# Kernel optimization log

Measured on AMD Instinct MI355X. Metric: run time of the kernel, lower is better.

## Reference

```python
import jax, jax.numpy as jnp
import numpy as np
import math

NUM_HEADS = 16
NUM_KV_HEADS = 4
HEAD_DIM = 128
HIDDEN = 2048
ROPE_BASE = 10000.0


def setup_inputs() -> dict:
    key = jax.random.key(0)
    ks = jax.random.split(key, 6)
    B, S = 1, 4096
    hidden_states = jax.random.normal(ks[0], (B, S, HIDDEN), dtype=jnp.float32)
    attention_mask = jnp.ones((B, S), dtype=jnp.int32)
    position_ids = jnp.broadcast_to(jnp.arange(S, dtype=jnp.int32)[None, :], (B, S))
    sc = 1.0 / math.sqrt(HIDDEN)
    wq = jax.random.normal(ks[1], (HIDDEN, NUM_HEADS * HEAD_DIM), dtype=jnp.float32) * sc
    wk = jax.random.normal(ks[2], (HIDDEN, NUM_KV_HEADS * HEAD_DIM), dtype=jnp.float32) * sc
    wv = jax.random.normal(ks[3], (HIDDEN, NUM_KV_HEADS * HEAD_DIM), dtype=jnp.float32) * sc
    wo = jax.random.normal(ks[4], (NUM_HEADS * HEAD_DIM, HIDDEN), dtype=jnp.float32) * sc
    return {"hidden_states": hidden_states, "attention_mask": attention_mask,
            "position_ids": position_ids, "wq": wq, "wk": wk, "wv": wv, "wo": wo}


def _rotate_half(x):
    x1, x2 = jnp.split(x, 2, axis=-1)
    return jnp.concatenate((-x2, x1), axis=-1)


def _rope_tables(seq_len, dtype):
    inv_freq = 1.0 / (ROPE_BASE ** (jnp.arange(0, HEAD_DIM, 2, dtype=jnp.float32) / HEAD_DIM))
    t = jnp.arange(seq_len, dtype=jnp.float32)
    freqs = jnp.outer(t, inv_freq)                       # [S, hd/2]
    emb = jnp.concatenate((freqs, freqs), axis=-1)       # [S, hd]
    return jnp.cos(emb).astype(dtype), jnp.sin(emb).astype(dtype)


def reference(hidden_states, attention_mask, position_ids, wq, wk, wv, wo):
    B, S, _ = hidden_states.shape
    dtype = hidden_states.dtype
    # projections -> [B, H, S, hd]
    q = (hidden_states @ wq).reshape(B, S, NUM_HEADS, HEAD_DIM).transpose(0, 2, 1, 3)
    k = (hidden_states @ wk).reshape(B, S, NUM_KV_HEADS, HEAD_DIM).transpose(0, 2, 1, 3)
    v = (hidden_states @ wv).reshape(B, S, NUM_KV_HEADS, HEAD_DIM).transpose(0, 2, 1, 3)
    # RoPE
    cos_t, sin_t = _rope_tables(S, dtype)
    cos = cos_t[position_ids][:, None]                   # [B,1,S,hd]
    sin = sin_t[position_ids][:, None]
    q = q * cos + _rotate_half(q) * sin
    k = k * cos + _rotate_half(k) * sin
    # GQA repeat
    n_rep = NUM_HEADS // NUM_KV_HEADS
    k = jnp.repeat(k, n_rep, axis=1)
    v = jnp.repeat(v, n_rep, axis=1)
    # scores + causal mask + padding mask
    scores = jnp.einsum('bhqd,bhkd->bhqk', q, k) / math.sqrt(HEAD_DIM)
    neg = jnp.finfo(scores.dtype).min
    causal = jnp.triu(jnp.full((S, S), neg, dtype=scores.dtype), k=1)
    scores = scores + causal[None, None]
    pad = (1.0 - attention_mask.astype(scores.dtype))[:, None, None, :] * neg
    scores = scores + pad
    attn = jax.nn.softmax(scores.astype(jnp.float32), axis=-1).astype(dtype)
    out = jnp.einsum('bhqk,bhkd->bhqd', attn, v)
    out = out.transpose(0, 2, 1, 3).reshape(B, S, NUM_HEADS * HEAD_DIM)
    return out @ wo
```

## Files before the change

kernel.cpp:

```cpp
#include <hip/hip_runtime.h>
#include <cstdint>
#include <cstddef>

typedef unsigned short ushort_t;
typedef short    bf16x8 __attribute__((ext_vector_type(8)));
typedef float    f32x4  __attribute__((ext_vector_type(4)));
typedef uint4    __attribute__((may_alias)) uint4_a;
typedef ushort4  __attribute__((may_alias)) ushort4_a;
typedef float4   __attribute__((may_alias)) float4_a;
typedef unsigned __attribute__((may_alias)) uint_a;

constexpr int SEQ = 4096, HID = 2048, NHEADS = 16, NKVH = 4, HDIM = 128;
constexpr int QD  = NHEADS * HDIM;
constexpr int KVD = NKVH * HDIM;
constexpr int KVL = 2 * KVD;

static __device__ __forceinline__ float bf2f(ushort_t u) {
    return __uint_as_float(((unsigned)u) << 16);
}
static __device__ __forceinline__ ushort_t f2bf(float f) {
    unsigned x = __float_as_uint(f);
    unsigned r = x + 0x7FFFu + ((x >> 16) & 1u);
    return (ushort_t)(r >> 16);
}
static __device__ __forceinline__ unsigned pack2(float lo, float hi) {
    return (unsigned)f2bf(lo) | ((unsigned)f2bf(hi) << 16);
}

static __device__ __forceinline__ void gld16(const ushort_t* g, ushort_t* l) {
    __builtin_amdgcn_global_load_lds(
        (const __attribute__((address_space(1))) unsigned*)g,
        (__attribute__((address_space(3))) unsigned*)l, 16, 0, 0);
}

__global__ __launch_bounds__(256) void cast_f32_bf16(
    const float* __restrict__ in, ushort_t* __restrict__ out, int n)
{
    int i = (blockIdx.x * 256 + threadIdx.x) * 8;
    if (i >= n) return;
    float4 a = *(const float4_a*)(in + i);
    float4 b = *(const float4_a*)(in + i + 4);
    uint4 o;
    o.x = pack2(a.x, a.y); o.y = pack2(a.z, a.w);
    o.z = pack2(b.x, b.y); o.w = pack2(b.z, b.w);
    *(uint4_a*)(out + i) = o;
}

__global__ __launch_bounds__(256) void transpose_cast(
    const float* __restrict__ W, ushort_t* __restrict__ WT, int K, int N)
{
    __shared__ float tl[32][36];
    const int k0 = blockIdx.x * 32, n0 = blockIdx.y * 32;
    const int t  = threadIdx.x;
    {
        int i = t >> 3, jb = (t & 7) * 4;
        *(float4_a*)&tl[i][jb] = *(const float4_a*)(W + (size_t)(k0 + i) * N + n0 + jb);
    }
    __syncthreads();
    {
        int n = t >> 3, kb = (t & 7) * 4;
        ushort4 o;
        o.x = f2bf(tl[kb + 0][n]); o.y = f2bf(tl[kb + 1][n]);
        o.z = f2bf(tl[kb + 2][n]); o.w = f2bf(tl[kb + 3][n]);
        *(ushort4_a*)(WT + (size_t)(n0 + n) * K + k0 + kb) = o;
    }
}

__global__ __launch_bounds__(256) void gemm_mfma(
    const ushort_t* __restrict__ A, int lda,
    const ushort_t* __restrict__ Bt, int ldb,
    void* __restrict__ C1, int ld1, void* __restrict__ C2, int ld2,
    int split, int N, int K, int out_f32)
{
    __shared__ ushort_t as[128 * 32];
    __shared__ ushort_t bs[128 * 32];

    const int t    = threadIdx.x;
    const int mb   = blockIdx.y * 128, nb = blockIdx.x * 128;
    const int w    = t >> 6, lane = t & 63, quad = lane >> 4, l15 = lane & 15;
    const int wm   = (w >> 1) * 64, wn = (w & 1) * 64;

    const int dr_row = lane >> 2, dr_c = lane & 3;
    const int rA0 = w * 16 + dr_row, rA1 = 64 + w * 16 + dr_row;
    const ushort_t* a0p = A  + (size_t)(mb + rA0) * lda + (dr_c ^ (rA0 & 3)) * 8;
    const ushort_t* a1p = A  + (size_t)(mb + rA1) * lda + (dr_c ^ (rA1 & 3)) * 8;
    const ushort_t* b0p = Bt + (size_t)(nb + rA0) * ldb + (dr_c ^ (rA0 & 3)) * 8;
    const ushort_t* b1p = Bt + (size_t)(nb + rA1) * ldb + (dr_c ^ (rA1 & 3)) * 8;
    ushort_t* asb0 = &as[(w) * 512];        ushort_t* asb1 = &as[(4 + w) * 512];
    ushort_t* bsb0 = &bs[(w) * 512];        ushort_t* bsb1 = &bs[(4 + w) * 512];

    f32x4 acc[4][4];
#pragma unroll
    for (int i = 0; i < 4; i++)
#pragma unroll
        for (int j = 0; j < 4; j++) acc[i][j] = (f32x4)0.f;

    const int chunk = quad ^ (l15 & 3);

    for (int kb = 0; kb < K; kb += 32) {
        __syncthreads();
        gld16(a0p + kb, asb0);
        gld16(a1p + kb, asb1);
        gld16(b0p + kb, bsb0);
        gld16(b1p + kb, bsb1);
        __syncthreads();

        bf16x8 af[4], bf[4];
#pragma unroll
        for (int mt = 0; mt < 4; mt++)
            af[mt] = *(const bf16x8*)&as[(wm + mt * 16 + l15) * 32 + chunk * 8];
#pragma unroll
        for (int nt = 0; nt < 4; nt++)
            bf[nt] = *(const bf16x8*)&bs[(wn + nt * 16 + l15) * 32 + chunk * 8];
#pragma unroll
        for (int mt = 0; mt < 4; mt++)
#pragma unroll
            for (int nt = 0; nt < 4; nt++)
                acc[mt][nt] = __builtin_amdgcn_mfma_f32_16x16x32_bf16(
                    af[mt], bf[nt], acc[mt][nt], 0, 0, 0);
    }

#pragma unroll
    for (int mt = 0; mt < 4; mt++)
#pragma unroll
        for (int nt = 0; nt < 4; nt++) {
            int colg = nb + wn + nt * 16 + l15;
#pragma unroll
            for (int r = 0; r < 4; r++) {
                int row = mb + wm + mt * 16 + quad * 4 + r;
                float v = acc[mt][nt][r];
                if (out_f32)            ((float*)C1)[(size_t)row * ld1 + colg] = v;
                else if (colg < split)  ((ushort_t*)C1)[(size_t)row * ld1 + colg] = f2bf(v);
                else                    ((ushort_t*)C2)[(size_t)row * ld2 + colg - split] = f2bf(v);
            }
        }
}

__global__ __launch_bounds__(256) void rope_bf16(
    ushort_t* __restrict__ buf, int ld, int nh, const int* __restrict__ pos_ids)
{
    int idx  = blockIdx.x * 256 + threadIdx.x;
    int i    = idx & 63;
    int rem  = idx >> 6;
    int head = rem % nh;
    int s    = rem / nh;
    if (s >= SEQ) return;

    float pos = (float)pos_ids[s];
    float ang = pos * __expf(-(float)i * 0.14391156831212787f);
    float c, sn;
    sincosf(ang, &sn, &c);

    ushort_t* p = buf + (size_t)s * ld + head * HDIM;
    float x0 = bf2f(p[i]);
    float x1 = bf2f(p[i + 64]);
    p[i]      = f2bf(x0 * c - x1 * sn);
    p[i + 64] = f2bf(x1 * c + x0 * sn);
}

__global__ __launch_bounds__(512, 4) void flash_mfma(
    const ushort_t* Q, const ushort_t* __restrict__ KV,
    const int* __restrict__ amask, ushort_t* O)
{
    __shared__ ushort_t ks[64][136];
    __shared__ ushort_t vt[128][72];
    __shared__ float    bias[64];

    const int t = threadIdx.x, w = t >> 6, lane = t & 63;
    const int quad = lane >> 4, l15 = lane & 15;
    const int h = blockIdx.x, kvh = h >> 2;
    const int q0 = (gridDim.y - 1 - blockIdx.y) * 128;
    const int q0w = q0 + w * 16;
    const int kcol = kvh * HDIM, vcol = KVD + kvh * HDIM;

    bf16x8 qf[4];
    {
        const ushort_t* qp = Q + (size_t)(q0w + l15) * QD + h * HDIM;
#pragma unroll
        for (int c = 0; c < 4; c++)
            qf[c] = *(const bf16x8*)(qp + c * 32 + quad * 8);
    }

    f32x4 accO[8];
#pragma unroll
    for (int j = 0; j < 8; j++) accO[j] = (f32x4)0.f;
    float m_s = -1e30f, l_s = 0.f;
    const float scale2 = 0.08838834764831845f * 1.44269504088896340f;

    const int krow = t >> 3,  kdo = (t & 7) * 16;
    const int vkp  = t & 31,  vdg = t >> 5;

    int bpi[4];
#pragma unroll
    for (int t4 = 0; t4 < 4; t4++)
        bpi[t4] = ((2 * (quad & 1) + (t4 >> 1)) * 16 + l15) * 4;
    const bool hi_half = (quad >> 1) != 0;

    uint4 kst[2], va, vb;
    float bst = 0.f;
    auto stage_load = [&](int kt) {
        const int k0 = kt * 64;
        const ushort_t* kp = KV + (size_t)(k0 + krow) * KVL + kcol + kdo;
        kst[0] = *(const uint4_a*)kp;
        kst[1] = *(const uint4_a*)(kp + 8);
        const ushort_t* vp = KV + (size_t)(k0 + 2 * vkp) * KVL + vcol + vdg * 8;
        va = *(const uint4_a*)vp;
        vb = *(const uint4_a*)(vp + KVL);
        if (t < 64) bst = amask[k0 + t] ? 0.f : -1e30f;
    };

    const int nkt = (q0 >> 6) + 2;
    stage_load(0);

    for (int kt = 0; kt < nkt; kt++) {
        const int k0 = kt * 64;
        __syncthreads();
        *(uint4_a*)&ks[krow][kdo]     = kst[0];
        *(uint4_a*)&ks[krow][kdo + 8] = kst[1];
        {
            unsigned aw[4] = {va.x, va.y, va.z, va.w};
            unsigned bw[4] = {vb.x, vb.y, vb.z, vb.w};
#pragma unroll
            for (int i = 0; i < 4; i++) {
                *(uint_a*)&vt[vdg * 8 + 2 * i][2 * vkp] =
                    (aw[i] & 0xFFFFu) | (bw[i] << 16);
                *(uint_a*)&vt[vdg * 8 + 2 * i + 1][2 * vkp] =
                    (aw[i] >> 16) | (bw[i] & 0xFFFF0000u);
            }
        }
        if (t < 64) bias[t] = bst;
        __syncthreads();
        if (kt + 1 < nkt) stage_load(kt + 1);

        if (k0 > q0w + 15) continue;

        f32x4 s[4];
#pragma unroll
        for (int mt = 0; mt < 4; mt++) s[mt] = (f32x4)0.f;
#pragma unroll
        for (int c = 0; c < 4; c++)
#pragma unroll
            for (int mt = 0; mt < 4; mt++) {
                bf16x8 kf = *(const bf16x8*)&ks[mt * 16 + l15][c * 32 + quad * 8];
                s[mt] = __builtin_amdgcn_mfma_f32_16x16x32_bf16(kf, qf[c], s[mt], 0, 0, 0);
            }

        const int qg = q0w + l15;
        const bool full = (k0 + 63 <= q0w);
        float p[4][4];
        float mx = -1e30f;
#pragma unroll
        for (int mt = 0; mt < 4; mt++) {
            float4 b4 = *(const float4_a*)&bias[mt * 16 + quad * 4];
            float br[4] = {b4.x, b4.y, b4.z, b4.w};
#pragma unroll
            for (int r = 0; r < 4; r++) {
                float v = fmaf(s[mt][r], scale2, br[r]);
                if (!full) {
                    int kg = k0 + mt * 16 + quad * 4 + r;
                    v = (kg > qg) ? -1e30f : v;
                }
                p[mt][r] = v;
                mx = fmaxf(mx, v);
            }
        }
        mx = fmaxf(mx, __shfl_xor(mx, 16));
        mx = fmaxf(mx, __shfl_xor(mx, 32));
        float mnew = fmaxf(m_s, mx);
        float alpha = exp2f(m_s - mnew);
        m_s = mnew;
        float sum = 0.f;
        unsigned wlo[4], whi[4];
#pragma unroll
        for (int mt = 0; mt < 4; mt++) {
            float p0 = exp2f(p[mt][0] - mnew);
            float p1 = exp2f(p[mt][1] - mnew);
            float p2 = exp2f(p[mt][2] - mnew);
            float p3 = exp2f(p[mt][3] - mnew);
            sum += (p0 + p1) + (p2 + p3);
            wlo[mt] = pack2(p0, p1);
            whi[mt] = pack2(p2, p3);
        }
        sum += __shfl_xor(sum, 16);
        sum += __shfl_xor(sum, 32);
        l_s = l_s * alpha + sum;

        {
            float a0 = __shfl(alpha, quad * 4 + 0);
            float a1 = __shfl(alpha, quad * 4 + 1);
            float a2 = __shfl(alpha, quad * 4 + 2);
            float a3 = __shfl(alpha, quad * 4 + 3);
#pragma unroll
            for (int j = 0; j < 8; j++) {
                f32x4 a = accO[j];
                a[0] *= a0; a[1] *= a1; a[2] *= a2; a[3] *= a3;
                accO[j] = a;
            }
        }

#pragma unroll
        for (int kc = 0; kc < 2; kc++) {
            union { unsigned u[4]; bf16x8 v; } pf;
#pragma unroll
            for (int t4 = 0; t4 < 4; t4++) {
                unsigned slo = (t4 & 1) ? whi[2 * kc]     : wlo[2 * kc];
                unsigned shi = (t4 & 1) ? whi[2 * kc + 1] : wlo[2 * kc + 1];
                int ra = __builtin_amdgcn_ds_bpermute(bpi[t4], (int)slo);
                int rb = __builtin_amdgcn_ds_bpermute(bpi[t4], (int)shi);
                pf.u[t4] = (unsigned)(hi_half ? rb : ra);
            }
#pragma unroll
            for (int n8 = 0; n8 < 8; n8++) {
                bf16x8 vf = *(const bf16x8*)&vt[n8 * 16 + l15][kc * 32 + quad * 8];
                accO[n8] = __builtin_amdgcn_mfma_f32_16x16x32_bf16(pf.v, vf, accO[n8], 0, 0, 0);
            }
        }
    }

    float linv = 1.0f / l_s;
#pragma unroll
    for (int r = 0; r < 4; r++) {
        float lr = __shfl(linv, quad * 4 + r);
        int row = q0w + quad * 4 + r;
        ushort_t* op = O + (size_t)row * QD + h * HDIM;
#pragma unroll
        for (int n8 = 0; n8 < 8; n8++)
            op[n8 * 16 + l15] = f2bf(accO[n8][r] * lr);
    }
}

extern "C" void kernel_launch(void* const* d_in, const int* in_sizes, int n_in,
                              void* d_out, int out_size, void* d_ws, size_t ws_size,
                              hipStream_t stream)
{
    const float* x     = (const float*)d_in[0];
    const int*   amask = (const int*)d_in[1];
    const int*   pos   = (const int*)d_in[2];
    const float* wq    = (const float*)d_in[3];
    const float* wk    = (const float*)d_in[4];
    const float* wv    = (const float*)d_in[5];
    const float* wo    = (const float*)d_in[6];
    float* out = (float*)d_out;

    ushort_t* wqkvT = (ushort_t*)d_out;
    ushort_t* xb    = wqkvT + (size_t)3072 * HID;

    ushort_t* qbuf  = (ushort_t*)d_ws;
    ushort_t* kvbuf = qbuf + (size_t)SEQ * QD;
    ushort_t* woT   = kvbuf;

    cast_f32_bf16<<<SEQ * HID / 8 / 256, 256, 0, stream>>>(x, xb, SEQ * HID);
    transpose_cast<<<dim3(HID / 32, QD / 32),  256, 0, stream>>>(wq, wqkvT, HID, QD);
    transpose_cast<<<dim3(HID / 32, KVD / 32), 256, 0, stream>>>(wk, wqkvT + (size_t)QD * HID, HID, KVD);
    transpose_cast<<<dim3(HID / 32, KVD / 32), 256, 0, stream>>>(wv, wqkvT + (size_t)(QD + KVD) * HID, HID, KVD);

    gemm_mfma<<<dim3(3072 / 128, SEQ / 128), 256, 0, stream>>>(
        xb, HID, wqkvT, HID, qbuf, QD, kvbuf, KVL, QD, 3072, HID, 0);

    rope_bf16<<<SEQ * NHEADS * 64 / 256, 256, 0, stream>>>(qbuf, QD, NHEADS, pos);
    rope_bf16<<<SEQ * NKVH  * 64 / 256, 256, 0, stream>>>(kvbuf, KVL, NKVH, pos);

    flash_mfma<<<dim3(NHEADS, SEQ / 128), 512, 0, stream>>>(qbuf, kvbuf, amask, qbuf);

    transpose_cast<<<dim3(QD / 32, HID / 32), 256, 0, stream>>>(wo, woT, QD, HID);
    gemm_mfma<<<dim3(HID / 128, SEQ / 128), 256, 0, stream>>>(
        qbuf, QD, woT, QD, out, HID, out, HID, HID, HID, QD, 1);
}
```

Before: 522.5 us.

## Restructure flash attention to 4 warps with 32 query rows each and 128-key tiles

```diff
diff --git a/kernel.cpp b/kernel.cpp
--- a/kernel.cpp
+++ b/kernel.cpp
@@ -158,174 +158,217 @@
     p[i + 64] = f2bf(x1 * c + x0 * sn);
 }
 
-__global__ __launch_bounds__(512, 4) void flash_mfma(
+__global__ __launch_bounds__(256, 2) void flash_mfma(
     const ushort_t* Q, const ushort_t* __restrict__ KV,
     const int* __restrict__ amask, ushort_t* O)
 {
-    __shared__ ushort_t ks[64][136];
-    __shared__ ushort_t vt[128][72];
-    __shared__ float    bias[64];
+    __shared__ ushort_t ks[128 * 128];
+    __shared__ ushort_t vt[128 * 128];
+    __shared__ float    bias[128];
 
     const int t = threadIdx.x, w = t >> 6, lane = t & 63;
     const int quad = lane >> 4, l15 = lane & 15;
     const int h = blockIdx.x, kvh = h >> 2;
     const int q0 = (gridDim.y - 1 - blockIdx.y) * 128;
-    const int q0w = q0 + w * 16;
+    const int q0w = q0 + w * 32;
     const int kcol = kvh * HDIM, vcol = KVD + kvh * HDIM;
 
-    bf16x8 qf[4];
-    {
-        const ushort_t* qp = Q + (size_t)(q0w + l15) * QD + h * HDIM;
+    bf16x8 qf[2][4];
+#pragma unroll
+    for (int nt = 0; nt < 2; nt++) {
+        const ushort_t* qp = Q + (size_t)(q0w + nt * 16 + l15) * QD + h * HDIM;
 #pragma unroll
         for (int c = 0; c < 4; c++)
-            qf[c] = *(const bf16x8*)(qp + c * 32 + quad * 8);
-    }
-
-    f32x4 accO[8];
-#pragma unroll
-    for (int j = 0; j < 8; j++) accO[j] = (f32x4)0.f;
-    float m_s = -1e30f, l_s = 0.f;
+            qf[nt][c] = *(const bf16x8*)(qp + c * 32 + quad * 8);
+    }
+
+    f32x4 accO[2][8];
+#pragma unroll
+    for (int i = 0; i < 2; i++)
+#pragma unroll
+        for (int j = 0; j < 8; j++) accO[i][j] = (f32x4)0.f;
+    float m_s[2] = {-1e30f, -1e30f}, l_s[2] = {0.f, 0.f};
     const float scale2 = 0.08838834764831845f * 1.44269504088896340f;
 
-    const int krow = t >> 3,  kdo = (t & 7) * 16;
-    const int vkp  = t & 31,  vdg = t >> 5;
-
-    int bpi[4];
-#pragma unroll
-    for (int t4 = 0; t4 < 4; t4++)
-        bpi[t4] = ((2 * (quad & 1) + (t4 >> 1)) * 16 + l15) * 4;
-    const bool hi_half = (quad >> 1) != 0;
-
-    uint4 kst[2], va, vb;
+    const int krow4 = t >> 4, kch = t & 15;
+    const int vkp   = t & 63, vdg = (t >> 6) * 32;
+
+    uint4 kst[8], va[4], vb[4];
     float bst = 0.f;
     auto stage_load = [&](int kt) {
-        const int k0 = kt * 64;
-        const ushort_t* kp = KV + (size_t)(k0 + krow) * KVL + kcol + kdo;
-        kst[0] = *(const uint4_a*)kp;
-        kst[1] = *(const uint4_a*)(kp + 8);
-        const ushort_t* vp = KV + (size_t)(k0 + 2 * vkp) * KVL + vcol + vdg * 8;
-        va = *(const uint4_a*)vp;
-        vb = *(const uint4_a*)(vp + KVL);
-        if (t < 64) bst = amask[k0 + t] ? 0.f : -1e30f;
+        const int k0 = kt * 128;
+#pragma unroll
+        for (int j = 0; j < 8; j++) {
+            int row = j * 16 + krow4;
+            kst[j] = *(const uint4_a*)(KV + (size_t)(k0 + row) * KVL + kcol + kch * 8);
+        }
+        const ushort_t* vp = KV + (size_t)(k0 + 2 * vkp) * KVL + vcol + vdg;
+#pragma unroll
+        for (int j = 0; j < 4; j++) {
+            va[j] = *(const uint4_a*)(vp + j * 8);
+            vb[j] = *(const uint4_a*)(vp + KVL + j * 8);
+        }
+        if (t < 128) bst = amask[k0 + t] ? 0.f : -1e30f;
     };
 
-    const int nkt = (q0 >> 6) + 2;
+    const int nkt = (q0 >> 7) + 1;
     stage_load(0);
 
     for (int kt = 0; kt < nkt; kt++) {
-        const int k0 = kt * 64;
+        const int k0 = kt * 128;
         __syncthreads();
-        *(uint4_a*)&ks[krow][kdo]     = kst[0];
-        *(uint4_a*)&ks[krow][kdo + 8] = kst[1];
+#pragma unroll
+        for (int j = 0; j < 8; j++) {
+            int row = j * 16 + krow4;
+            int pc  = kch ^ (row & 7);
+            *(uint4_a*)&ks[row * 128 + pc * 8] = kst[j];
+        }
         {
-            unsigned aw[4] = {va.x, va.y, va.z, va.w};
-            unsigned bw[4] = {vb.x, vb.y, vb.z, vb.w};
-#pragma unroll
-            for (int i = 0; i < 4; i++) {
-                *(uint_a*)&vt[vdg * 8 + 2 * i][2 * vkp] =
-                    (aw[i] & 0xFFFFu) | (bw[i] << 16);
-                *(uint_a*)&vt[vdg * 8 + 2 * i + 1][2 * vkp] =
-                    (aw[i] >> 16) | (bw[i] & 0xFFFF0000u);
-            }
-        }
-        if (t < 64) bias[t] = bst;
+            unsigned ua[16] = {va[0].x, va[0].y, va[0].z, va[0].w,
+                               va[1].x, va[1].y, va[1].z, va[1].w,
+                               va[2].x, va[2].y, va[2].z, va[2].w,
+                               va[3].x, va[3].y, va[3].z, va[3].w};
+            unsigned ub[16] = {vb[0].x, vb[0].y, vb[0].z, vb[0].w,
+                               vb[1].x, vb[1].y, vb[1].z, vb[1].w,
+                               vb[2].x, vb[2].y, vb[2].z, vb[2].w,
+                               vb[3].x, vb[3].y, vb[3].z, vb[3].w};
+            const int coff = 2 * (vkp & 3), cch = vkp >> 2;
+#pragma unroll
+            for (int j = 0; j < 16; j++) {
+                int d0 = vdg + 2 * j, d1 = d0 + 1;
+                *(uint_a*)&vt[d0 * 128 + (cch ^ (d0 & 7)) * 8 + coff] =
+                    (ua[j] & 0xFFFFu) | (ub[j] << 16);
+                *(uint_a*)&vt[d1 * 128 + (cch ^ (d1 & 7)) * 8 + coff] =
+                    (ua[j] >> 16) | (ub[j] & 0xFFFF0000u);
+            }
+        }
+        if (t < 128) bias[t] = bst;
         __syncthreads();
         if (kt + 1 < nkt) stage_load(kt + 1);
 
-        if (k0 > q0w + 15) continue;
-
-        f32x4 s[4];
-#pragma unroll
-        for (int mt = 0; mt < 4; mt++) s[mt] = (f32x4)0.f;
-#pragma unroll
-        for (int c = 0; c < 4; c++)
+#pragma unroll
+        for (int sub = 0; sub < 2; sub++) {
+            const int kb = k0 + sub * 64;
+            f32x4 s[4][2];
+#pragma unroll
+            for (int mt = 0; mt < 4; mt++)
+#pragma unroll
+                for (int nt = 0; nt < 2; nt++) s[mt][nt] = (f32x4)0.f;
+#pragma unroll
+            for (int c = 0; c < 4; c++)
+#pragma unroll
+                for (int mt = 0; mt < 4; mt++) {
+                    int row = sub * 64 + mt * 16 + l15;
+                    int pc  = (4 * c + quad) ^ (l15 & 7);
+                    bf16x8 kf = *(const bf16x8*)&ks[row * 128 + pc * 8];
+#pragma unroll
+                    for (int nt = 0; nt < 2; nt++)
+                        s[mt][nt] = __builtin_amdgcn_mfma_f32_16x16x32_bf16(
+                            kf, qf[nt][c], s[mt][nt], 0, 0, 0);
+                }
+
+            float br[4][4];
 #pragma unroll
             for (int mt = 0; mt < 4; mt++) {
-                bf16x8 kf = *(const bf16x8*)&ks[mt * 16 + l15][c * 32 + quad * 8];
-                s[mt] = __builtin_amdgcn_mfma_f32_16x16x32_bf16(kf, qf[c], s[mt], 0, 0, 0);
-            }
-
-        const int qg = q0w + l15;
-        const bool full = (k0 + 63 <= q0w);
-        float p[4][4];
-        float mx = -1e30f;
-#pragma unroll
-        for (int mt = 0; mt < 4; mt++) {
-            float4 b4 = *(const float4_a*)&bias[mt * 16 + quad * 4];
-            float br[4] = {b4.x, b4.y, b4.z, b4.w};
-#pragma unroll
-            for (int r = 0; r < 4; r++) {
-                float v = fmaf(s[mt][r], scale2, br[r]);
-                if (!full) {
-                    int kg = k0 + mt * 16 + quad * 4 + r;
-                    v = (kg > qg) ? -1e30f : v;
+                float4 b4 = *(const float4_a*)&bias[sub * 64 + mt * 16 + quad * 4];
+                br[mt][0] = b4.x; br[mt][1] = b4.y; br[mt][2] = b4.z; br[mt][3] = b4.w;
+            }
+
+            float alpha[2];
+            unsigned wlo[2][4], whi[2][4];
+#pragma unroll
+            for (int nt = 0; nt < 2; nt++) {
+                const int qg = q0w + nt * 16 + l15;
+                const bool full = (kb + 63 <= q0w + nt * 16);
+                float vals[4][4];
+                float mx = -1e30f;
+#pragma unroll
+                for (int mt = 0; mt < 4; mt++)
+#pragma unroll
+                    for (int r = 0; r < 4; r++) {
+                        float v = fmaf(s[mt][nt][r], scale2, br[mt][r]);
+                        if (!full) {
+                            int kg = kb + mt * 16 + quad * 4 + r;
+                            v = (kg > qg) ? -1e30f : v;
+                        }
+                        vals[mt][r] = v;
+                        mx = fmaxf(mx, v);
+                    }
+                mx = fmaxf(mx, __shfl_xor(mx, 16));
+                mx = fmaxf(mx, __shfl_xor(mx, 32));
+                float mnew = fmaxf(m_s[nt], mx);
+                alpha[nt] = exp2f(m_s[nt] - mnew);
+                m_s[nt] = mnew;
+                float sum = 0.f;
+#pragma unroll
+                for (int mt = 0; mt < 4; mt++) {
+                    float p0 = exp2f(vals[mt][0] - mnew);
+                    float p1 = exp2f(vals[mt][1] - mnew);
+                    float p2 = exp2f(vals[mt][2] - mnew);
+                    float p3 = exp2f(vals[mt][3] - mnew);
+                    sum += (p0 + p1) + (p2 + p3);
+                    wlo[nt][mt] = pack2(p0, p1);
+                    whi[nt][mt] = pack2(p2, p3);
                 }
-                p[mt][r] = v;
-                mx = fmaxf(mx, v);
-            }
-        }
-        mx = fmaxf(mx, __shfl_xor(mx, 16));
-        mx = fmaxf(mx, __shfl_xor(mx, 32));
-        float mnew = fmaxf(m_s, mx);
-        float alpha = exp2f(m_s - mnew);
-        m_s = mnew;
-        float sum = 0.f;
-        unsigned wlo[4], whi[4];
-#pragma unroll
-        for (int mt = 0; mt < 4; mt++) {
-            float p0 = exp2f(p[mt][0] - mnew);
-            float p1 = exp2f(p[mt][1] - mnew);
-            float p2 = exp2f(p[mt][2] - mnew);
-            float p3 = exp2f(p[mt][3] - mnew);
-            sum += (p0 + p1) + (p2 + p3);
-            wlo[mt] = pack2(p0, p1);
-            whi[mt] = pack2(p2, p3);
-        }
-        sum += __shfl_xor(sum, 16);
-        sum += __shfl_xor(sum, 32);
-        l_s = l_s * alpha + sum;
-
-        {
-            float a0 = __shfl(alpha, quad * 4 + 0);
-            float a1 = __shfl(alpha, quad * 4 + 1);
-            float a2 = __shfl(alpha, quad * 4 + 2);
-            float a3 = __shfl(alpha, quad * 4 + 3);
-#pragma unroll
-            for (int j = 0; j < 8; j++) {
-                f32x4 a = accO[j];
-                a[0] *= a0; a[1] *= a1; a[2] *= a2; a[3] *= a3;
-                accO[j] = a;
-            }
-        }
-
-#pragma unroll
-        for (int kc = 0; kc < 2; kc++) {
-            union { unsigned u[4]; bf16x8 v; } pf;
-#pragma unroll
-            for (int t4 = 0; t4 < 4; t4++) {
-                unsigned slo = (t4 & 1) ? whi[2 * kc]     : wlo[2 * kc];
-                unsigned shi = (t4 & 1) ? whi[2 * kc + 1] : wlo[2 * kc + 1];
-                int ra = __builtin_amdgcn_ds_bpermute(bpi[t4], (int)slo);
-                int rb = __builtin_amdgcn_ds_bpermute(bpi[t4], (int)shi);
-                pf.u[t4] = (unsigned)(hi_half ? rb : ra);
-            }
-#pragma unroll
-            for (int n8 = 0; n8 < 8; n8++) {
-                bf16x8 vf = *(const bf16x8*)&vt[n8 * 16 + l15][kc * 32 + quad * 8];
-                accO[n8] = __builtin_amdgcn_mfma_f32_16x16x32_bf16(pf.v, vf, accO[n8], 0, 0, 0);
-            }
-        }
-    }
-
-    float linv = 1.0f / l_s;
-#pragma unroll
-    for (int r = 0; r < 4; r++) {
-        float lr = __shfl(linv, quad * 4 + r);
-        int row = q0w + quad * 4 + r;
-        ushort_t* op = O + (size_t)row * QD + h * HDIM;
-#pragma unroll
-        for (int n8 = 0; n8 < 8; n8++)
-            op[n8 * 16 + l15] = f2bf(accO[n8][r] * lr);
+                sum += __shfl_xor(sum, 16);
+                sum += __shfl_xor(sum, 32);
+                l_s[nt] = l_s[nt] * alpha[nt] + sum;
+            }
+
+#pragma unroll
+            for (int nt = 0; nt < 2; nt++) {
+                float a0 = __shfl(alpha[nt], quad * 4 + 0);
+                float a1 = __shfl(alpha[nt], quad * 4 + 1);
+                float a2 = __shfl(alpha[nt], quad * 4 + 2);
+                float a3 = __shfl(alpha[nt], quad * 4 + 3);
+#pragma unroll
+                for (int j = 0; j < 8; j++) {
+                    f32x4 a = accO[nt][j];
+                    a[0] *= a0; a[1] *= a1; a[2] *= a2; a[3] *= a3;
+                    accO[nt][j] = a;
+                }
+            }
+
+#pragma unroll
+            for (int kc = 0; kc < 2; kc++) {
+                union { unsigned u[4]; bf16x8 v; } pf[2];
+#pragma unroll
+                for (int nt = 0; nt < 2; nt++)
+#pragma unroll
+                    for (int t4 = 0; t4 < 4; t4++) {
+                        int bpi = ((2 * (quad & 1) + (t4 >> 1)) * 16 + l15) * 4;
+                        unsigned slo = (t4 & 1) ? whi[nt][2 * kc]     : wlo[nt][2 * kc];
+                        unsigned shi = (t4 & 1) ? whi[nt][2 * kc + 1] : wlo[nt][2 * kc + 1];
+                        int ra = __builtin_amdgcn_ds_bpermute(bpi, (int)slo);
+                        int rb = __builtin_amdgcn_ds_bpermute(bpi, (int)shi);
+                        pf[nt].u[t4] = (unsigned)((quad >> 1) ? rb : ra);
+                    }
+#pragma unroll
+                for (int n8 = 0; n8 < 8; n8++) {
+                    int row = n8 * 16 + l15;
+                    int pc  = (sub * 8 + 4 * kc + quad) ^ (l15 & 7);
+                    bf16x8 vf = *(const bf16x8*)&vt[row * 128 + pc * 8];
+#pragma unroll
+                    for (int nt = 0; nt < 2; nt++)
+                        accO[nt][n8] = __builtin_amdgcn_mfma_f32_16x16x32_bf16(
+                            pf[nt].v, vf, accO[nt][n8], 0, 0, 0);
+                }
+            }
+        }
+    }
+
+#pragma unroll
+    for (int nt = 0; nt < 2; nt++) {
+        float linv = 1.0f / l_s[nt];
+#pragma unroll
+        for (int r = 0; r < 4; r++) {
+            float lr = __shfl(linv, quad * 4 + r);
+            int row = q0w + nt * 16 + quad * 4 + r;
+            ushort_t* op = O + (size_t)row * QD + h * HDIM;
+#pragma unroll
+            for (int n8 = 0; n8 < 8; n8++)
+                op[n8 * 16 + l15] = f2bf(accO[nt][n8][r] * lr);
+        }
     }
 }
 
@@ -360,7 +403,7 @@
     rope_bf16<<<SEQ * NHEADS * 64 / 256, 256, 0, stream>>>(qbuf, QD, NHEADS, pos);
     rope_bf16<<<SEQ * NKVH  * 64 / 256, 256, 0, stream>>>(kvbuf, KVL, NKVH, pos);
 
-    flash_mfma<<<dim3(NHEADS, SEQ / 128), 512, 0, stream>>>(qbuf, kvbuf, amask, qbuf);
+    flash_mfma<<<dim3(NHEADS, SEQ / 128), 256, 0, stream>>>(qbuf, kvbuf, amask, qbuf);
 
     transpose_cast<<<dim3(QD / 32, HID / 32), 256, 0, stream>>>(wo, woT, QD, HID);
     gemm_mfma<<<dim3(HID / 128, SEQ / 128), 256, 0, stream>>>(
```

Result: slower. 660.9 us (+26.5%).
